# Kernel optimization log

Measured on AMD Instinct MI355X. Metric: run time of the kernel, lower is better.

The kernel has to match this reference:

```python
import jax, jax.numpy as jnp
import numpy as np

B, H, W, C = 128, 224, 224, 3
FLAT = (H // 4) * (W // 4) * 10  # 31360 after two 2x2 maxpools on 10-ch conv


def _conv_relu(x, w, b):
    y = jax.lax.conv_general_dilated(
        x, w, window_strides=(1, 1), padding='SAME',
        dimension_numbers=('NHWC', 'HWIO', 'NHWC'))
    return jax.nn.relu(y + b)


def _maxpool2(x):
    return jax.lax.reduce_window(x, -jnp.inf, jax.lax.max,
                                 (1, 2, 2, 1), (1, 2, 2, 1), 'VALID')


def setup_inputs() -> dict:
    key = jax.random.key(0)
    ks = jax.random.split(key, 9)
    identity_bias = jnp.array([1., 0., 0., 0., 1., 0.], jnp.float32)
    return {
        'x': jax.random.uniform(ks[0], (B, H, W, C), jnp.float32),
        'conv1_w': jax.random.normal(ks[1], (3, 3, C, 8), jnp.float32) * 0.1,
        'conv1_b': jnp.zeros((8,), jnp.float32),
        'conv2_w': jax.random.normal(ks[2], (3, 3, 8, 10), jnp.float32) * 0.1,
        'conv2_b': jnp.zeros((10,), jnp.float32),
        'fc1_w': jax.random.normal(ks[3], (FLAT, 32), jnp.float32) * 0.01,
        'fc1_b': jnp.zeros((32,), jnp.float32),
        'fc2_w': jax.random.normal(ks[4], (32, 6), jnp.float32) * 0.01,
        'fc2_b': identity_bias,
    }


def reference(x, conv1_w, conv1_b, conv2_w, conv2_b, fc1_w, fc1_b, fc2_w, fc2_b):
    b, h, w, c = x.shape
    # --- localization network ---
    t = _maxpool2(_conv_relu(x, conv1_w, conv1_b))
    t = _maxpool2(_conv_relu(t, conv2_w, conv2_b))
    t = t.reshape(b, -1)
    t = jax.nn.relu(t @ fc1_w + fc1_b)
    theta = (t @ fc2_w + fc2_b).reshape(b, 2, 3)
    # --- affine grid generation ---
    xs = jnp.linspace(-1.0, 1.0, w)
    ys = jnp.linspace(-1.0, 1.0, h)
    xt, yt = jnp.meshgrid(xs, ys)                 # [H,W]
    base = jnp.stack([xt, yt, jnp.ones_like(xt)], axis=-1)  # [H,W,3]
    grid = jnp.einsum('bkj,hwj->bhwk', theta, base)          # [B,H,W,2]
    # --- bilinear sampling ---
    x_s = (grid[..., 0] + 1.0) * 0.5 * (w - 1.0)
    y_s = (grid[..., 1] + 1.0) * 0.5 * (h - 1.0)
    x0 = jnp.clip(jnp.floor(x_s).astype(jnp.int32), 0, w - 1)
    x1 = jnp.clip(x0 + 1, 0, w - 1)
    y0 = jnp.clip(jnp.floor(y_s).astype(jnp.int32), 0, h - 1)
    y1 = jnp.clip(y0 + 1, 0, h - 1)
    bidx = jnp.arange(b)[:, None, None]
    I00 = x[bidx, y0, x0]  # [B,H,W,C]
    I01 = x[bidx, y1, x0]
    I10 = x[bidx, y0, x1]
    I11 = x[bidx, y1, x1]
    x0f, x1f = x0.astype(x.dtype), x1.astype(x.dtype)
    y0f, y1f = y0.astype(x.dtype), y1.astype(x.dtype)
    wa = ((x1f - x_s) * (y1f - y_s))[..., None]
    wb = ((x1f - x_s) * (y_s - y0f))[..., None]
    wc = ((x_s - x0f) * (y1f - y_s))[..., None]
    wd = ((x_s - x0f) * (y_s - y0f))[..., None]
    return wa * I00 + wb * I01 + wc * I10 + wd * I11
```

## Files before the change

### kernel.cpp

```cpp
#include <hip/hip_runtime.h>

#define BATCH 128
#define H 224
#define W 224
#define PH1 112
#define PH2 56
#define FLAT (PH2*PH2*10)
#define KC 64

__global__ __launch_bounds__(256) void k_conv1(const float* __restrict__ x,
        const float* __restrict__ w, const float* __restrict__ bias,
        float* __restrict__ pool1) {
    __shared__ float ws[216];
    __shared__ float bs[8];
    int tid = threadIdx.x;
    if (tid < 216) ws[tid] = w[tid];
    if (tid < 8) bs[tid] = bias[tid];
    __syncthreads();
    int gid = blockIdx.x * 256 + tid;
    int pw = gid % PH1;
    int t2 = gid / PH1;
    int ph = t2 % PH1;
    int b  = t2 / PH1;

    float in[4][4][3];
    #pragma unroll
    for (int r = 0; r < 4; ++r) {
        int iy = 2*ph - 1 + r;
        bool yok = (iy >= 0) && (iy < H);
        #pragma unroll
        for (int cpx = 0; cpx < 4; ++cpx) {
            int ix = 2*pw - 1 + cpx;
            bool ok = yok && (ix >= 0) && (ix < W);
            const float* p = x + ((size_t)((b*H + iy)*W + ix))*3;
            in[r][cpx][0] = ok ? p[0] : 0.f;
            in[r][cpx][1] = ok ? p[1] : 0.f;
            in[r][cpx][2] = ok ? p[2] : 0.f;
        }
    }
    float pooled[8];
    #pragma unroll
    for (int co = 0; co < 8; ++co) pooled[co] = 0.f;

    #pragma unroll
    for (int cy = 0; cy < 2; ++cy)
    #pragma unroll
    for (int cx = 0; cx < 2; ++cx) {
        float acc[8];
        #pragma unroll
        for (int co = 0; co < 8; ++co) acc[co] = bs[co];
        #pragma unroll
        for (int ky = 0; ky < 3; ++ky)
        #pragma unroll
        for (int kx = 0; kx < 3; ++kx)
        #pragma unroll
        for (int ci = 0; ci < 3; ++ci) {
            float v = in[cy+ky][cx+kx][ci];
            const float* wp = &ws[((ky*3+kx)*3+ci)*8];
            #pragma unroll
            for (int co = 0; co < 8; ++co) acc[co] = fmaf(v, wp[co], acc[co]);
        }
        #pragma unroll
        for (int co = 0; co < 8; ++co) pooled[co] = fmaxf(pooled[co], acc[co]);
    }
    float4* o4 = (float4*)(pool1 + (size_t)gid*8);
    o4[0] = make_float4(pooled[0], pooled[1], pooled[2], pooled[3]);
    o4[1] = make_float4(pooled[4], pooled[5], pooled[6], pooled[7]);
}

#define C2_ROWS 10
#define C2_COLS 114
#define C2_PLANE (C2_ROWS*C2_COLS)
__global__ __launch_bounds__(256) void k_conv2(const float* __restrict__ pool1,
        const float* __restrict__ w, const float* __restrict__ bias,
        float* __restrict__ pool2) {
    __shared__ float lds[8*C2_PLANE];
    __shared__ float ws[720];
    __shared__ float bs[10];
    int tid = threadIdx.x;
    int rg = blockIdx.x % 14;
    int b  = blockIdx.x / 14;

    for (int i = tid; i < 720; i += 256) ws[i] = w[i];
    if (tid < 10) bs[tid] = bias[tid];
    if (tid < 160) {
        int ci = tid / 20, rem = tid % 20;
        int r = rem >> 1, col = (rem & 1) ? (C2_COLS-1) : 0;
        lds[ci*C2_PLANE + r*C2_COLS + col] = 0.f;
    }
    int row0 = 8*rg - 1;
    for (int i = tid; i < 2240; i += 256) {
        int r = i / 224, rem = i % 224;
        int pix = rem >> 1, half = rem & 1;
        int iy = row0 + r;
        float4 v = make_float4(0.f,0.f,0.f,0.f);
        if (iy >= 0 && iy < PH1)
            v = *(const float4*)(pool1 + ((size_t)((b*PH1 + iy)*PH1 + pix))*8 + half*4);
        float* dst = lds + (half*4)*C2_PLANE + r*C2_COLS + (pix+1);
        dst[0*C2_PLANE] = v.x;
        dst[1*C2_PLANE] = v.y;
        dst[2*C2_PLANE] = v.z;
        dst[3*C2_PLANE] = v.w;
    }
    __syncthreads();

    if (tid >= 224) return;
    int dpr = tid / 56, pc = tid % 56;
    int rbase = 2*dpr;
    int cbase = 2*pc;

    float acc[4][10];
    #pragma unroll
    for (int p = 0; p < 4; ++p)
        #pragma unroll
        for (int co = 0; co < 10; ++co) acc[p][co] = bs[co];

    #pragma unroll
    for (int ci = 0; ci < 8; ++ci) {
        float v[4][4];
        #pragma unroll
        for (int r = 0; r < 4; ++r) {
            const float2* lp2 = (const float2*)(lds + ci*C2_PLANE + (rbase+r)*C2_COLS + cbase);
            float2 a = lp2[0], c = lp2[1];
            v[r][0] = a.x; v[r][1] = a.y; v[r][2] = c.x; v[r][3] = c.y;
        }
        #pragma unroll
        for (int ky = 0; ky < 3; ++ky)
        #pragma unroll
        for (int kx = 0; kx < 3; ++kx) {
            const float* wp = &ws[((ky*3+kx)*8+ci)*10];
            float wv[10];
            #pragma unroll
            for (int co = 0; co < 10; ++co) wv[co] = wp[co];
            #pragma unroll
            for (int cy = 0; cy < 2; ++cy)
            #pragma unroll
            for (int cx = 0; cx < 2; ++cx) {
                float vv = v[cy+ky][cx+kx];
                #pragma unroll
                for (int co = 0; co < 10; ++co)
                    acc[cy*2+cx][co] = fmaf(vv, wv[co], acc[cy*2+cx][co]);
            }
        }
    }

    float pooled[10];
    #pragma unroll
    for (int co = 0; co < 10; ++co)
        pooled[co] = fmaxf(fmaxf(fmaxf(fmaxf(0.f, acc[0][co]), acc[1][co]), acc[2][co]), acc[3][co]);
    int pr = 4*rg + dpr;
    float2* o2 = (float2*)(pool2 + ((size_t)(b*PH2 + pr)*PH2 + pc)*10);
    #pragma unroll
    for (int i = 0; i < 5; ++i) o2[i] = make_float2(pooled[2*i], pooled[2*i+1]);
}

__global__ __launch_bounds__(256) void k_fc1(const float* __restrict__ pool2,
        const float* __restrict__ w, float* __restrict__ t_raw) {
    __shared__ float Ash[BATCH][KC];
    __shared__ float Wsh[KC][32];
    int tid = threadIdx.x;
    int k0 = blockIdx.x * KC;
    for (int i = tid; i < KC*32; i += 256) {
        int k = i >> 5, n = i & 31;
        Wsh[k][n] = w[(size_t)(k0 + k)*32 + n];
    }
    {
        int k = tid & 63, br = tid >> 6;
        for (int p = 0; p < 32; ++p) {
            int b = p*4 + br;
            Ash[b][k] = pool2[(size_t)b*FLAT + k0 + k];
        }
    }
    __syncthreads();
    int n = tid & 31, bg = tid >> 5;
    for (int bo = 0; bo < 16; ++bo) {
        int b = bo*8 + bg;
        float acc = 0.f;
        #pragma unroll
        for (int k = 0; k < KC; ++k) acc = fmaf(Ash[b][k], Wsh[k][n], acc);
        atomicAdd(&t_raw[b*32 + n], acc);
    }
}

__global__ __launch_bounds__(128) void k_fc2(const float* __restrict__ t_raw,
        const float* __restrict__ fc1_b,
        const float* __restrict__ w, const float* __restrict__ bias,
        float* __restrict__ theta) {
    int b = threadIdx.x;
    float acc[6];
    #pragma unroll
    for (int j = 0; j < 6; ++j) acc[j] = bias[j];
    for (int i = 0; i < 32; ++i) {
        float t = fmaxf(t_raw[b*32 + i] + fc1_b[i], 0.f);
        #pragma unroll
        for (int j = 0; j < 6; ++j) acc[j] = fmaf(t, w[i*6 + j], acc[j]);
    }
    #pragma unroll
    for (int j = 0; j < 6; ++j) theta[b*6 + j] = acc[j];
}

__global__ __launch_bounds__(256) void k_sample(const float* __restrict__ x,
        const float* __restrict__ theta, float* __restrict__ out) {
    int gid = blockIdx.x * 256 + threadIdx.x;
    int wi = gid % W;
    int t2 = gid / W;
    int hi = t2 % H;
    int b  = t2 / H;
    const float* th = theta + b*6;
    float xt = -1.0f + wi * (2.0f/223.0f);
    float yt = -1.0f + hi * (2.0f/223.0f);
    float gx = th[0]*xt + th[1]*yt + th[2];
    float gy = th[3]*xt + th[4]*yt + th[5];
    float x_s = (gx + 1.0f) * 0.5f * 223.0f;
    float y_s = (gy + 1.0f) * 0.5f * 223.0f;
    int x0 = min(max((int)floorf(x_s), 0), W-1);
    int x1 = min(x0 + 1, W-1);
    int y0 = min(max((int)floorf(y_s), 0), H-1);
    int y1 = min(y0 + 1, H-1);
    float x0f = (float)x0, x1f = (float)x1, y0f = (float)y0, y1f = (float)y1;
    float wa = (x1f - x_s) * (y1f - y_s);
    float wb = (x1f - x_s) * (y_s - y0f);
    float wc = (x_s - x0f) * (y1f - y_s);
    float wd = (x_s - x0f) * (y_s - y0f);
    const float* base = x + (size_t)b*H*W*3;
    const float* p00 = base + (size_t)(y0*W + x0)*3;
    const float* p01 = base + (size_t)(y1*W + x0)*3;
    const float* p10 = base + (size_t)(y0*W + x1)*3;
    const float* p11 = base + (size_t)(y1*W + x1)*3;
    float* o = out + (size_t)gid*3;
    #pragma unroll
    for (int c = 0; c < 3; ++c)
        o[c] = wa*p00[c] + wb*p01[c] + wc*p10[c] + wd*p11[c];
}

extern "C" void kernel_launch(void* const* d_in, const int* in_sizes, int n_in,
                              void* d_out, int out_size, void* d_ws, size_t ws_size,
                              hipStream_t stream) {
    const float* x       = (const float*)d_in[0];
    const float* conv1_w = (const float*)d_in[1];
    const float* conv1_b = (const float*)d_in[2];
    const float* conv2_w = (const float*)d_in[3];
    const float* conv2_b = (const float*)d_in[4];
    const float* fc1_w   = (const float*)d_in[5];
    const float* fc1_b   = (const float*)d_in[6];
    const float* fc2_w   = (const float*)d_in[7];
    const float* fc2_b   = (const float*)d_in[8];
    float* out = (float*)d_out;

    float* pool1 = out;
    float* pool2 = out + 12845056;
    float* t_raw = (float*)d_ws;
    float* theta = t_raw + BATCH*32;

    hipMemsetAsync(t_raw, 0, BATCH*32*sizeof(float), stream);
    k_conv1<<<6272, 256, 0, stream>>>(x, conv1_w, conv1_b, pool1);
    k_conv2<<<1792, 256, 0, stream>>>(pool1, conv2_w, conv2_b, pool2);
    k_fc1<<<490, 256, 0, stream>>>(pool2, fc1_w, t_raw);
    k_fc2<<<1, 128, 0, stream>>>(t_raw, fc1_b, fc2_w, fc2_b, theta);
    k_sample<<<25088, 256, 0, stream>>>(x, theta, out);
}
```

Before: 146.4 us.

## Stage conv1 input rows in LDS as planar tiles with coalesced float4 loads

Conv1 now gives each block 2 pooled rows of one image. The block loads the 6 input rows it needs with coalesced float4 reads and transposes them into planar LDS with a zero halo, so each thread no longer does 48 scattered scalar global loads. Weights are read directly from global memory, which should hit the scalar cache, instead of being staged in LDS. The pooling logic is also reorganised so that all four conv outputs are accumulated at once. In exchange, 32 of the 256 threads in each block sit idle, the LDS writes during the transpose may hit bank conflicts, and the grid grows to 7168 blocks.

New measurement: 164.0 us. +12.0%, slower.

```diff
diff --git a/kernel.cpp b/kernel.cpp
--- a/kernel.cpp
+++ b/kernel.cpp
@@ -8,62 +8,86 @@
 #define FLAT (PH2*PH2*10)
 #define KC 64
 
+#define C1R 6
+#define C1C 228
 __global__ __launch_bounds__(256) void k_conv1(const float* __restrict__ x,
         const float* __restrict__ w, const float* __restrict__ bias,
         float* __restrict__ pool1) {
-    __shared__ float ws[216];
-    __shared__ float bs[8];
+    __shared__ float lds[3*C1R*C1C];
     int tid = threadIdx.x;
-    if (tid < 216) ws[tid] = w[tid];
-    if (tid < 8) bs[tid] = bias[tid];
+    int rg = blockIdx.x % 56;
+    int b  = blockIdx.x / 56;
+
+    if (tid < 72) {
+        int ch = tid / 24, rem = tid % 24;
+        int r = rem / 4, c4 = rem % 4;
+        int col = (c4 == 0) ? 0 : (224 + c4);
+        lds[(ch*C1R + r)*C1C + col] = 0.f;
+    }
+    int row0 = 4*rg - 1;
+    const float* xb = x + (size_t)b*H*W*3;
+    for (int i = tid; i < 1008; i += 256) {
+        int r = i / 168, f4 = i % 168;
+        int iy = row0 + r;
+        float4 v = make_float4(0.f,0.f,0.f,0.f);
+        if (iy >= 0 && iy < H)
+            v = *(const float4*)(xb + (size_t)iy*672 + f4*4);
+        int fl = f4*4;
+        float vv[4] = {v.x, v.y, v.z, v.w};
+        #pragma unroll
+        for (int c = 0; c < 4; ++c) {
+            int f = fl + c;
+            int px = f / 3, ch = f - 3*px;
+            lds[(ch*C1R + r)*C1C + (px+1)] = vv[c];
+        }
+    }
     __syncthreads();
-    int gid = blockIdx.x * 256 + tid;
-    int pw = gid % PH1;
-    int t2 = gid / PH1;
-    int ph = t2 % PH1;
-    int b  = t2 / PH1;
-
-    float in[4][4][3];
-    #pragma unroll
-    for (int r = 0; r < 4; ++r) {
-        int iy = 2*ph - 1 + r;
-        bool yok = (iy >= 0) && (iy < H);
-        #pragma unroll
-        for (int cpx = 0; cpx < 4; ++cpx) {
-            int ix = 2*pw - 1 + cpx;
-            bool ok = yok && (ix >= 0) && (ix < W);
-            const float* p = x + ((size_t)((b*H + iy)*W + ix))*3;
-            in[r][cpx][0] = ok ? p[0] : 0.f;
-            in[r][cpx][1] = ok ? p[1] : 0.f;
-            in[r][cpx][2] = ok ? p[2] : 0.f;
-        }
-    }
+
+    if (tid >= 224) return;
+    int dpr = tid >> 7, pc = tid & 127;
+    dpr = tid / 112; pc = tid % 112;
+
+    float acc[4][8];
+    #pragma unroll
+    for (int p = 0; p < 4; ++p)
+        #pragma unroll
+        for (int co = 0; co < 8; ++co) acc[p][co] = bias[co];
+
+    #pragma unroll
+    for (int ci = 0; ci < 3; ++ci) {
+        float v[4][4];
+        #pragma unroll
+        for (int rr = 0; rr < 4; ++rr) {
+            const float2* lp2 = (const float2*)(lds + ((size_t)(ci*C1R + 2*dpr + rr))*C1C + 2*pc);
+            float2 a = lp2[0], c2 = lp2[1];
+            v[rr][0] = a.x; v[rr][1] = a.y; v[rr][2] = c2.x; v[rr][3] = c2.y;
+        }
+        #pragma unroll
+        for (int ky = 0; ky < 3; ++ky)
+        #pragma unroll
+        for (int kx = 0; kx < 3; ++kx) {
+            const float* wp = &w[((ky*3+kx)*3+ci)*8];
+            float wv[8];
+            #pragma unroll
+            for (int co = 0; co < 8; ++co) wv[co] = wp[co];
+            #pragma unroll
+            for (int cy = 0; cy < 2; ++cy)
+            #pragma unroll
+            for (int cx = 0; cx < 2; ++cx) {
+                float vin = v[cy+ky][cx+kx];
+                #pragma unroll
+                for (int co = 0; co < 8; ++co)
+                    acc[cy*2+cx][co] = fmaf(vin, wv[co], acc[cy*2+cx][co]);
+            }
+        }
+    }
+
     float pooled[8];
     #pragma unroll
-    for (int co = 0; co < 8; ++co) pooled[co] = 0.f;
-
-    #pragma unroll
-    for (int cy = 0; cy < 2; ++cy)
-    #pragma unroll
-    for (int cx = 0; cx < 2; ++cx) {
-        float acc[8];
-        #pragma unroll
-        for (int co = 0; co < 8; ++co) acc[co] = bs[co];
-        #pragma unroll
-        for (int ky = 0; ky < 3; ++ky)
-        #pragma unroll
-        for (int kx = 0; kx < 3; ++kx)
-        #pragma unroll
-        for (int ci = 0; ci < 3; ++ci) {
-            float v = in[cy+ky][cx+kx][ci];
-            const float* wp = &ws[((ky*3+kx)*3+ci)*8];
-            #pragma unroll
-            for (int co = 0; co < 8; ++co) acc[co] = fmaf(v, wp[co], acc[co]);
-        }
-        #pragma unroll
-        for (int co = 0; co < 8; ++co) pooled[co] = fmaxf(pooled[co], acc[co]);
-    }
-    float4* o4 = (float4*)(pool1 + (size_t)gid*8);
+    for (int co = 0; co < 8; ++co)
+        pooled[co] = fmaxf(fmaxf(fmaxf(fmaxf(0.f, acc[0][co]), acc[1][co]), acc[2][co]), acc[3][co]);
+    int pr = 2*rg + dpr;
+    float4* o4 = (float4*)(pool1 + ((size_t)((b*PH1 + pr)*PH1 + pc))*8);
     o4[0] = make_float4(pooled[0], pooled[1], pooled[2], pooled[3]);
     o4[1] = make_float4(pooled[4], pooled[5], pooled[6], pooled[7]);
 }
@@ -253,7 +277,7 @@
     float* theta = t_raw + BATCH*32;
 
     hipMemsetAsync(t_raw, 0, BATCH*32*sizeof(float), stream);
-    k_conv1<<<6272, 256, 0, stream>>>(x, conv1_w, conv1_b, pool1);
+    k_conv1<<<7168, 256, 0, stream>>>(x, conv1_w, conv1_b, pool1);
     k_conv2<<<1792, 256, 0, stream>>>(pool1, conv2_w, conv2_b, pool2);
     k_fc1<<<490, 256, 0, stream>>>(pool2, fc1_w, t_raw);
     k_fc2<<<1, 128, 0, stream>>>(t_raw, fc1_b, fc2_w, fc2_b, theta);
```
